# Kernel tuning notes

Hardware: AMD Instinct MI355X
Metric: run time of the kernel (lower is better)

## Reference

```python
import jax, jax.numpy as jnp
import numpy as np
from jax import lax

B, T, EPROJS, DUNITS, ATT_DIM = 32, 2048, 1024, 1024, 512
ACONV_CHANS, ACONV_FILTS = 32, 15
SCALING = 2.0


def setup_inputs() -> dict:
    key = jax.random.key(0)
    ks = jax.random.split(key, 12)
    enc_hs_pad = jax.random.normal(ks[0], (B, T, EPROJS), dtype=jnp.float32)
    enc_hs_len = jax.random.randint(ks[1], (B,), T // 2, T + 1, dtype=jnp.int32)
    dec_z = jax.random.normal(ks[2], (B, DUNITS), dtype=jnp.float32)
    ap = jax.random.uniform(ks[3], (B, T), dtype=jnp.float32)
    att_prev = ap / jnp.sum(ap, axis=1, keepdims=True)  # previous attention distribution
    # parameters (PyTorch Linear: y = x @ W^T + b; stored here pre-transposed as [in, out])
    s_enc = 1.0 / np.sqrt(EPROJS)
    s_dec = 1.0 / np.sqrt(DUNITS)
    s_att = 1.0 / np.sqrt(ACONV_CHANS)
    s_g = 1.0 / np.sqrt(ATT_DIM)
    K = 2 * ACONV_FILTS + 1
    s_c = 1.0 / np.sqrt(K)
    W_enc = jax.random.uniform(ks[4], (EPROJS, ATT_DIM), jnp.float32, -s_enc, s_enc)
    b_enc = jax.random.uniform(ks[5], (ATT_DIM,), jnp.float32, -s_enc, s_enc)
    W_dec = jax.random.uniform(ks[6], (DUNITS, ATT_DIM), jnp.float32, -s_dec, s_dec)
    W_att = jax.random.uniform(ks[7], (ACONV_CHANS, ATT_DIM), jnp.float32, -s_att, s_att)
    conv_w = jax.random.uniform(ks[8], (ACONV_CHANS, 1, K), jnp.float32, -s_c, s_c)
    W_g = jax.random.uniform(ks[9], (ATT_DIM, 1), jnp.float32, -s_g, s_g)
    b_g = jax.random.uniform(ks[10], (1,), jnp.float32, -s_g, s_g)
    return {"enc_hs_pad": enc_hs_pad, "enc_hs_len": enc_hs_len, "dec_z": dec_z,
            "att_prev": att_prev, "W_enc": W_enc, "b_enc": b_enc, "W_dec": W_dec,
            "W_att": W_att, "conv_w": conv_w, "W_g": W_g, "b_g": b_g}


def reference(enc_hs_pad, enc_hs_len, dec_z, att_prev,
              W_enc, b_enc, W_dec, W_att, conv_w, W_g, b_g):
    # pre-computed encoder projection: (B, T, A)
    pre_enc = jnp.einsum('btd,da->bta', enc_hs_pad, W_enc) + b_enc
    # location conv over previous attention: (B, 1, T) -> (B, C, T), SAME padding
    pad = (conv_w.shape[-1] - 1) // 2
    att_conv = lax.conv_general_dilated(
        att_prev[:, None, :], conv_w, window_strides=(1,),
        padding=[(pad, pad)], dimension_numbers=('NCH', 'OIH', 'NCH'))
    att_c = jnp.einsum('bct,ca->bta', att_conv, W_att)       # (B, T, A)
    dec_t = (dec_z @ W_dec)[:, None, :]                       # (B, 1, A)
    # energies: (B, T)
    e = jnp.einsum('bta,ao->bt', jnp.tanh(att_c + pre_enc + dec_t), W_g) + b_g[0]
    # pad mask: True where t >= length
    mask = jnp.arange(e.shape[1])[None, :] >= enc_hs_len[:, None]
    e = jnp.where(mask, -jnp.inf, e)
    w = jax.nn.softmax(SCALING * e, axis=1)                   # (B, T)
    c = jnp.einsum('btd,bt->bd', enc_hs_pad, w)               # (B, EPROJS)
    return c, w
```

## Files before the change

### kernel.cpp

```cpp
#include <hip/hip_runtime.h>
#include <stdint.h>

#define T_LEN 2048
#define KAUG  1056
#define M_TOT 65536

typedef __attribute__((ext_vector_type(8))) short short8;
typedef __attribute__((ext_vector_type(4))) float f32x4;
typedef unsigned int u32;
typedef unsigned short u16;

__device__ __forceinline__ u16 bf16_rn(float f){
  u32 u = __builtin_bit_cast(u32, f);
  u32 r = u + 0x7fffu + ((u >> 16) & 1u);
  return (u16)(r >> 16);
}
__device__ __forceinline__ u32 pack_trunc(float lo, float hi){
  u32 a = __builtin_bit_cast(u32, lo);
  u32 b = __builtin_bit_cast(u32, hi);
  return (a >> 16) | (b & 0xffff0000u);
}
__device__ __forceinline__ void lds_load16(const void* g, void* l){
  __builtin_amdgcn_global_load_lds(
      (const __attribute__((address_space(1))) u32*)g,
      (__attribute__((address_space(3))) u32*)l, 16, 0, 0);
}

__global__ void k_build_bt(const float* __restrict__ W_enc,
                           const float* __restrict__ W_att,
                           u16* __restrict__ Bt){
  __shared__ float tile[32][33];
  int k0 = blockIdx.x * 32, n0 = blockIdx.y * 32;
  int tx = threadIdx.x & 31, ty = threadIdx.x >> 5;
  #pragma unroll
  for (int i = 0; i < 4; i++){
    int k = k0 + i*8 + ty;
    int n = n0 + tx;
    float v = (k < 1024) ? W_enc[k*512 + n] : W_att[(k-1024)*512 + n];
    tile[i*8+ty][tx] = v;
  }
  __syncthreads();
  #pragma unroll
  for (int i = 0; i < 4; i++){
    int n = n0 + i*8 + ty;
    int k = k0 + tx;
    Bt[(size_t)n*KAUG + k] = bf16_rn(tile[tx][i*8+ty]);
  }
}

__global__ void k_bias(const float* __restrict__ dec_z,
                       const float* __restrict__ W_dec,
                       const float* __restrict__ b_enc,
                       float* __restrict__ bias){
  __shared__ float red[4][64];
  int b = blockIdx.y, n0 = blockIdx.x * 64;
  int nl = threadIdx.x & 63, ks = threadIdx.x >> 6;
  int n = n0 + nl;
  const float* dz = dec_z + b*1024;
  float s = 0.f;
  #pragma unroll 4
  for (int k = ks*256; k < ks*256 + 256; k++) s += dz[k] * W_dec[k*512 + n];
  red[ks][nl] = s;
  __syncthreads();
  if (threadIdx.x < 64){
    int nn = n0 + threadIdx.x;
    bias[b*512 + nn] = b_enc[nn] + red[0][threadIdx.x] + red[1][threadIdx.x]
                     + red[2][threadIdx.x] + red[3][threadIdx.x];
  }
}

__global__ void k_conv(const float* __restrict__ att_prev,
                       const float* __restrict__ conv_w,
                       float* __restrict__ attT){
  int idx = blockIdx.x*256 + threadIdx.x;
  int c = idx & 31;
  int bt = idx >> 5;
  int b = bt >> 11, t = bt & 2047;
  const float* ap = att_prev + b*2048;
  const float* cw = conv_w + c*31;
  float s = 0.f;
  #pragma unroll
  for (int j = 0; j < 31; j++){
    int tt = t + j - 15;
    float a = (tt >= 0 && tt < 2048) ? ap[tt] : 0.f;
    s += cw[j] * a;
  }
  attT[(size_t)bt*32 + c] = s;
}

__launch_bounds__(256)
__global__ void k_gemm_energy(const float* __restrict__ enc,
                              const float* __restrict__ attT,
                              const u16* __restrict__ Bt,
                              const float* __restrict__ bias,
                              const float* __restrict__ Wg,
                              float* __restrict__ ePart){
  __shared__ float Ash[128*32];
  __shared__ u16   Bsh[128*32];
  __shared__ float eRed[2][128];

  const int tid  = threadIdx.x;
  const int lane = tid & 63;
  const int wid  = tid >> 6;
  const int wave_m = wid >> 1, wave_n = wid & 1;
  const int bidx = blockIdx.x;
  const int xcd  = bidx & 7;
  const int s_sq = bidx >> 3;
  const int nblk = s_sq & 3;
  const int mblk = ((s_sq >> 2) << 3) + xcd;
  const int row0 = mblk << 7;
  const int b    = mblk >> 4;

  f32x4 acc[4][4];
  #pragma unroll
  for (int i = 0; i < 4; i++)
    #pragma unroll
    for (int j = 0; j < 4; j++) acc[i][j] = (f32x4)(0.f);

  const int arow_in = lane >> 3;
  const int ap_phys = lane & 7;
  const int brow_in = lane >> 2;
  const int bp_phys = lane & 3;
  const int fr_m = lane & 15;
  const int kg   = lane >> 4;

  const u16* BtN = Bt + (size_t)(nblk*128)*KAUG;

  #pragma unroll 1
  for (int kk = 0; kk < 33; ++kk){
    const float* srcA; int rstr;
    if (kk < 32){ srcA = enc  + (size_t)row0*1024 + kk*32; rstr = 1024; }
    else        { srcA = attT + (size_t)row0*32;           rstr = 32;   }
    #pragma unroll
    for (int q = 0; q < 4; q++){
      int r = wid*32 + q*8 + arow_in;
      int c = ap_phys ^ (r & 7);
      lds_load16(srcA + (size_t)r*rstr + c*4, Ash + (wid*32 + q*8)*32);
    }
    const u16* srcB = BtN + kk*32;
    #pragma unroll
    for (int q = 0; q < 2; q++){
      int n = wid*32 + q*16 + brow_in;
      int c = bp_phys ^ ((n >> 1) & 3);
      lds_load16(srcB + (size_t)n*KAUG + c*8, Bsh + (wid*32 + q*16)*32);
    }
    __syncthreads();

    short8 afrag[4], bfrag[4];
    #pragma unroll
    for (int mi = 0; mi < 4; mi++){
      int m  = wave_m*64 + mi*16 + fr_m;
      int c0 = kg*2;
      int p0 = c0 ^ (m & 7), p1 = (c0+1) ^ (m & 7);
      const f32x4* rowp = (const f32x4*)(Ash + m*32);
      f32x4 x0 = rowp[p0];
      f32x4 x1 = rowp[p1];
      union { u32 u[4]; short8 s; } cv;
      cv.u[0] = pack_trunc(x0.x, x0.y);
      cv.u[1] = pack_trunc(x0.z, x0.w);
      cv.u[2] = pack_trunc(x1.x, x1.y);
      cv.u[3] = pack_trunc(x1.z, x1.w);
      afrag[mi] = cv.s;
    }
    #pragma unroll
    for (int ni = 0; ni < 4; ni++){
      int n = wave_n*64 + ni*16 + fr_m;
      int p = kg ^ ((n >> 1) & 3);
      bfrag[ni] = *(const short8*)(Bsh + n*32 + p*8);
    }
    #pragma unroll
    for (int mi = 0; mi < 4; mi++)
      #pragma unroll
      for (int ni = 0; ni < 4; ni++)
        acc[mi][ni] = __builtin_amdgcn_mfma_f32_16x16x32_bf16(afrag[mi], bfrag[ni], acc[mi][ni], 0, 0, 0);

    __syncthreads();
  }

  float wg[4], bs[4];
  #pragma unroll
  for (int ni = 0; ni < 4; ni++){
    int ng = nblk*128 + wave_n*64 + ni*16 + fr_m;
    wg[ni] = Wg[ng];
    bs[ni] = bias[b*512 + ng];
  }
  #pragma unroll
  for (int mi = 0; mi < 4; mi++){
    #pragma unroll
    for (int reg = 0; reg < 4; reg++){
      float s = 0.f;
      #pragma unroll
      for (int ni = 0; ni < 4; ni++){
        float v  = acc[mi][ni][reg] + bs[ni];
        float e2 = __expf(2.f * v);
        float th = 1.f - 2.f/(e2 + 1.f);
        s += wg[ni] * th;
      }
      s += __shfl_xor(s, 1);
      s += __shfl_xor(s, 2);
      s += __shfl_xor(s, 4);
      s += __shfl_xor(s, 8);
      if (fr_m == 0){
        int rowl = wave_m*64 + mi*16 + kg*4 + reg;
        eRed[wave_n][rowl] = s;
      }
    }
  }
  __syncthreads();
  if (tid < 128)
    ePart[(size_t)nblk*M_TOT + row0 + tid] = eRed[0][tid] + eRed[1][tid];
}

__global__ void k_softmax(const float* __restrict__ ePart,
                          const int* __restrict__ lens,
                          float* __restrict__ wout){
  int b = blockIdx.x, tid = threadIdx.x;
  int lane = tid & 63, wid = tid >> 6;
  int len = lens[b];
  __shared__ float red[4];
  float x[8]; float m = -3.0e38f;
  #pragma unroll
  for (int i = 0; i < 8; i++){
    int t = tid + i*256;
    int idx = b*2048 + t;
    float e = ePart[idx] + ePart[M_TOT + idx] + ePart[2*M_TOT + idx] + ePart[3*M_TOT + idx];
    float xx = (t < len) ? 2.0f*e : -3.0e38f;
    x[i] = xx; m = fmaxf(m, xx);
  }
  #pragma unroll
  for (int o = 1; o < 64; o <<= 1) m = fmaxf(m, __shfl_xor(m, o));
  if (lane == 0) red[wid] = m;
  __syncthreads();
  m = fmaxf(fmaxf(red[0], red[1]), fmaxf(red[2], red[3]));
  float s = 0.f;
  #pragma unroll
  for (int i = 0; i < 8; i++){
    float ex = (x[i] > -1.0e38f) ? __expf(x[i] - m) : 0.f;
    x[i] = ex; s += ex;
  }
  #pragma unroll
  for (int o = 1; o < 64; o <<= 1) s += __shfl_xor(s, o);
  __syncthreads();
  if (lane == 0) red[wid] = s;
  __syncthreads();
  s = red[0] + red[1] + red[2] + red[3];
  float inv = 1.0f / s;
  #pragma unroll
  for (int i = 0; i < 8; i++){
    int t = tid + i*256;
    wout[b*2048 + t] = x[i]*inv;
  }
}

__global__ void k_ctx_partial(const float* __restrict__ enc,
                              const float* __restrict__ w,
                              float* __restrict__ cPart){
  int dc = blockIdx.x, tc = blockIdx.y, b = blockIdx.z;
  int d = dc*256 + threadIdx.x;
  const float* ep = enc + ((size_t)(b*2048 + tc*256))*1024 + d;
  const float* wp = w + b*2048 + tc*256;
  float s0 = 0, s1 = 0, s2 = 0, s3 = 0;
  #pragma unroll 2
  for (int t = 0; t < 256; t += 4){
    s0 += wp[t+0] * ep[(size_t)(t+0)*1024];
    s1 += wp[t+1] * ep[(size_t)(t+1)*1024];
    s2 += wp[t+2] * ep[(size_t)(t+2)*1024];
    s3 += wp[t+3] * ep[(size_t)(t+3)*1024];
  }
  cPart[((size_t)tc*32 + b)*1024 + d] = (s0 + s1) + (s2 + s3);
}

__global__ void k_ctx_reduce(const float* __restrict__ cPart, float* __restrict__ cOut){
  int idx = blockIdx.x*256 + threadIdx.x;
  float s = 0.f;
  #pragma unroll
  for (int tc = 0; tc < 8; tc++) s += cPart[tc*32768 + idx];
  cOut[idx] = s;
}

extern "C" void kernel_launch(void* const* d_in, const int* in_sizes, int n_in,
                              void* d_out, int out_size, void* d_ws, size_t ws_size,
                              hipStream_t stream){
  (void)in_sizes; (void)n_in; (void)out_size; (void)ws_size;
  const float* enc    = (const float*)d_in[0];
  const int*   lens   = (const int*)  d_in[1];
  const float* dec_z  = (const float*)d_in[2];
  const float* att_p  = (const float*)d_in[3];
  const float* W_enc  = (const float*)d_in[4];
  const float* b_enc  = (const float*)d_in[5];
  const float* W_dec  = (const float*)d_in[6];
  const float* W_att  = (const float*)d_in[7];
  const float* conv_w = (const float*)d_in[8];
  const float* W_g    = (const float*)d_in[9];

  char* ws = (char*)d_ws;
  u16*   Bt    = (u16*)  (ws);
  float* attT  = (float*)(ws + 1081344);
  float* bias  = (float*)(ws + 1081344 + 8388608);
  float* ePart = (float*)(ws + 1081344 + 8388608 + 65536);
  float* cPart = (float*)(ws + 1081344 + 8388608 + 65536 + 1048576);

  float* c_out = (float*)d_out;
  float* w_out = c_out + 32*1024;

  hipLaunchKernelGGL(k_build_bt,    dim3(33,16),  dim3(256), 0, stream, W_enc, W_att, Bt);
  hipLaunchKernelGGL(k_bias,        dim3(8,32),   dim3(256), 0, stream, dec_z, W_dec, b_enc, bias);
  hipLaunchKernelGGL(k_conv,        dim3(8192),   dim3(256), 0, stream, att_p, conv_w, attT);
  hipLaunchKernelGGL(k_gemm_energy, dim3(2048),   dim3(256), 0, stream, enc, attT, Bt, bias, W_g, ePart);
  hipLaunchKernelGGL(k_softmax,     dim3(32),     dim3(256), 0, stream, ePart, lens, w_out);
  hipLaunchKernelGGL(k_ctx_partial, dim3(4,8,32), dim3(256), 0, stream, enc, w_out, cPart);
  hipLaunchKernelGGL(k_ctx_reduce,  dim3(128),    dim3(256), 0, stream, cPart, c_out);
}
```

Measured before the change: 594.3 us.

## Pre-convert encoder states to bf16 and fuse conv features into augmented rows

Adds a pass that converts the encoder tensor to bf16 into a workspace buffer, with the location-conv outputs written into the extra 32 columns of each row. The GEMM then stages bf16 A tiles directly via LDS loads instead of loading f32 and truncating per fragment. The context kernel is vectorized to float4 with more time chunks. This adds an extra full read/write pass over the encoder tensor and requires a large workspace, falling back to the old f32 path otherwise.

After: 655.2 us. +10.3%, slower.

```diff
diff --git a/kernel.cpp b/kernel.cpp
--- a/kernel.cpp
+++ b/kernel.cpp
@@ -3,6 +3,7 @@
 
 #define T_LEN 2048
 #define KAUG  1056
+#define ROWB  1056
 #define M_TOT 65536
 
 typedef __attribute__((ext_vector_type(8))) short short8;
@@ -44,7 +45,7 @@
   for (int i = 0; i < 4; i++){
     int n = n0 + i*8 + ty;
     int k = k0 + tx;
-    Bt[(size_t)n*KAUG + k] = bf16_rn(tile[tx][i*8+ty]);
+    Bt[(size_t)n*ROWB + k] = bf16_rn(tile[tx][i*8+ty]);
   }
 }
 
@@ -69,9 +70,20 @@
   }
 }
 
-__global__ void k_conv(const float* __restrict__ att_prev,
-                       const float* __restrict__ conv_w,
-                       float* __restrict__ attT){
+__global__ void k_cvt(const float* __restrict__ enc, u16* __restrict__ encB){
+  int g = blockIdx.x*256 + threadIdx.x;
+  int bt = g >> 7, kx = (g & 127) << 3;
+  const f32x4* in = (const f32x4*)(enc + (size_t)bt*1024 + kx);
+  f32x4 a = in[0], b = in[1];
+  union { u16 h[8]; uint4 v; } o;
+  o.h[0]=bf16_rn(a.x); o.h[1]=bf16_rn(a.y); o.h[2]=bf16_rn(a.z); o.h[3]=bf16_rn(a.w);
+  o.h[4]=bf16_rn(b.x); o.h[5]=bf16_rn(b.y); o.h[6]=bf16_rn(b.z); o.h[7]=bf16_rn(b.w);
+  *(uint4*)(encB + (size_t)bt*ROWB + kx) = o.v;
+}
+
+__global__ void k_conv_bf16(const float* __restrict__ att_prev,
+                            const float* __restrict__ conv_w,
+                            u16* __restrict__ encB){
   int idx = blockIdx.x*256 + threadIdx.x;
   int c = idx & 31;
   int bt = idx >> 5;
@@ -85,18 +97,36 @@
     float a = (tt >= 0 && tt < 2048) ? ap[tt] : 0.f;
     s += cw[j] * a;
   }
+  encB[(size_t)bt*ROWB + 1024 + c] = bf16_rn(s);
+}
+
+__global__ void k_conv_f32(const float* __restrict__ att_prev,
+                           const float* __restrict__ conv_w,
+                           float* __restrict__ attT){
+  int idx = blockIdx.x*256 + threadIdx.x;
+  int c = idx & 31;
+  int bt = idx >> 5;
+  int b = bt >> 11, t = bt & 2047;
+  const float* ap = att_prev + b*2048;
+  const float* cw = conv_w + c*31;
+  float s = 0.f;
+  #pragma unroll
+  for (int j = 0; j < 31; j++){
+    int tt = t + j - 15;
+    float a = (tt >= 0 && tt < 2048) ? ap[tt] : 0.f;
+    s += cw[j] * a;
+  }
   attT[(size_t)bt*32 + c] = s;
 }
 
 __launch_bounds__(256)
-__global__ void k_gemm_energy(const float* __restrict__ enc,
-                              const float* __restrict__ attT,
-                              const u16* __restrict__ Bt,
-                              const float* __restrict__ bias,
-                              const float* __restrict__ Wg,
-                              float* __restrict__ ePart){
-  __shared__ float Ash[128*32];
-  __shared__ u16   Bsh[128*32];
+__global__ void k_gemm_bf16(const u16* __restrict__ encB,
+                            const u16* __restrict__ Bt,
+                            const float* __restrict__ bias,
+                            const float* __restrict__ Wg,
+                            float* __restrict__ ePart){
+  __shared__ u16 Ash[128*32];
+  __shared__ u16 Bsh[128*32];
   __shared__ float eRed[2][128];
 
   const int tid  = threadIdx.x;
@@ -117,50 +147,32 @@
     #pragma unroll
     for (int j = 0; j < 4; j++) acc[i][j] = (f32x4)(0.f);
 
-  const int arow_in = lane >> 3;
-  const int ap_phys = lane & 7;
-  const int brow_in = lane >> 2;
-  const int bp_phys = lane & 3;
+  const int r_in = lane >> 2;
+  const int phys = lane & 3;
   const int fr_m = lane & 15;
   const int kg   = lane >> 4;
 
-  const u16* BtN = Bt + (size_t)(nblk*128)*KAUG;
+  const u16* Abase = encB + (size_t)row0*ROWB;
+  const u16* Bbase = Bt + (size_t)(nblk*128)*ROWB;
 
   #pragma unroll 1
   for (int kk = 0; kk < 33; ++kk){
-    const float* srcA; int rstr;
-    if (kk < 32){ srcA = enc  + (size_t)row0*1024 + kk*32; rstr = 1024; }
-    else        { srcA = attT + (size_t)row0*32;           rstr = 32;   }
-    #pragma unroll
-    for (int q = 0; q < 4; q++){
-      int r = wid*32 + q*8 + arow_in;
-      int c = ap_phys ^ (r & 7);
-      lds_load16(srcA + (size_t)r*rstr + c*4, Ash + (wid*32 + q*8)*32);
-    }
-    const u16* srcB = BtN + kk*32;
+    const int k0 = kk*32;
     #pragma unroll
     for (int q = 0; q < 2; q++){
-      int n = wid*32 + q*16 + brow_in;
-      int c = bp_phys ^ ((n >> 1) & 3);
-      lds_load16(srcB + (size_t)n*KAUG + c*8, Bsh + (wid*32 + q*16)*32);
+      int r = q*64 + wid*16 + r_in;
+      int c = phys ^ ((r >> 1) & 3);
+      lds_load16(Abase + (size_t)r*ROWB + k0 + c*8, Ash + (q*64 + wid*16)*32);
+      lds_load16(Bbase + (size_t)r*ROWB + k0 + c*8, Bsh + (q*64 + wid*16)*32);
     }
     __syncthreads();
 
     short8 afrag[4], bfrag[4];
     #pragma unroll
     for (int mi = 0; mi < 4; mi++){
-      int m  = wave_m*64 + mi*16 + fr_m;
-      int c0 = kg*2;
-      int p0 = c0 ^ (m & 7), p1 = (c0+1) ^ (m & 7);
-      const f32x4* rowp = (const f32x4*)(Ash + m*32);
-      f32x4 x0 = rowp[p0];
-      f32x4 x1 = rowp[p1];
-      union { u32 u[4]; short8 s; } cv;
-      cv.u[0] = pack_trunc(x0.x, x0.y);
-      cv.u[1] = pack_trunc(x0.z, x0.w);
-      cv.u[2] = pack_trunc(x1.x, x1.y);
-      cv.u[3] = pack_trunc(x1.z, x1.w);
-      afrag[mi] = cv.s;
+      int m = wave_m*64 + mi*16 + fr_m;
+      int p = kg ^ ((m >> 1) & 3);
+      afrag[mi] = *(const short8*)(Ash + m*32 + p*8);
     }
     #pragma unroll
     for (int ni = 0; ni < 4; ni++){
@@ -211,6 +223,129 @@
     ePart[(size_t)nblk*M_TOT + row0 + tid] = eRed[0][tid] + eRed[1][tid];
 }
 
+__launch_bounds__(256)
+__global__ void k_gemm_f32(const float* __restrict__ enc,
+                           const float* __restrict__ attT,
+                           const u16* __restrict__ Bt,
+                           const float* __restrict__ bias,
+                           const float* __restrict__ Wg,
+                           float* __restrict__ ePart){
+  __shared__ float Ash[128*32];
+  __shared__ u16   Bsh[128*32];
+  __shared__ float eRed[2][128];
+
+  const int tid  = threadIdx.x;
+  const int lane = tid & 63;
+  const int wid  = tid >> 6;
+  const int wave_m = wid >> 1, wave_n = wid & 1;
+  const int bidx = blockIdx.x;
+  const int xcd  = bidx & 7;
+  const int s_sq = bidx >> 3;
+  const int nblk = s_sq & 3;
+  const int mblk = ((s_sq >> 2) << 3) + xcd;
+  const int row0 = mblk << 7;
+  const int b    = mblk >> 4;
+
+  f32x4 acc[4][4];
+  #pragma unroll
+  for (int i = 0; i < 4; i++)
+    #pragma unroll
+    for (int j = 0; j < 4; j++) acc[i][j] = (f32x4)(0.f);
+
+  const int arow_in = lane >> 3;
+  const int ap_phys = lane & 7;
+  const int brow_in = lane >> 2;
+  const int bp_phys = lane & 3;
+  const int fr_m = lane & 15;
+  const int kg   = lane >> 4;
+
+  const u16* BtN = Bt + (size_t)(nblk*128)*ROWB;
+
+  #pragma unroll 1
+  for (int kk = 0; kk < 33; ++kk){
+    const float* srcA; int rstr;
+    if (kk < 32){ srcA = enc  + (size_t)row0*1024 + kk*32; rstr = 1024; }
+    else        { srcA = attT + (size_t)row0*32;           rstr = 32;   }
+    #pragma unroll
+    for (int q = 0; q < 4; q++){
+      int r = wid*32 + q*8 + arow_in;
+      int c = ap_phys ^ (r & 7);
+      lds_load16(srcA + (size_t)r*rstr + c*4, Ash + (wid*32 + q*8)*32);
+    }
+    const u16* srcB = BtN + kk*32;
+    #pragma unroll
+    for (int q = 0; q < 2; q++){
+      int n = wid*32 + q*16 + brow_in;
+      int c = bp_phys ^ ((n >> 1) & 3);
+      lds_load16(srcB + (size_t)n*ROWB + c*8, Bsh + (wid*32 + q*16)*32);
+    }
+    __syncthreads();
+
+    short8 afrag[4], bfrag[4];
+    #pragma unroll
+    for (int mi = 0; mi < 4; mi++){
+      int m  = wave_m*64 + mi*16 + fr_m;
+      int c0 = kg*2;
+      int p0 = c0 ^ (m & 7), p1 = (c0+1) ^ (m & 7);
+      const f32x4* rowp = (const f32x4*)(Ash + m*32);
+      f32x4 x0 = rowp[p0];
+      f32x4 x1 = rowp[p1];
+      union { u32 u[4]; short8 s; } cv;
+      cv.u[0] = pack_trunc(x0.x, x0.y);
+      cv.u[1] = pack_trunc(x0.z, x0.w);
+      cv.u[2] = pack_trunc(x1.x, x1.y);
+      cv.u[3] = pack_trunc(x1.z, x1.w);
+      afrag[mi] = cv.s;
+    }
+    #pragma unroll
+    for (int ni = 0; ni < 4; ni++){
+      int n = wave_n*64 + ni*16 + fr_m;
+      int p = kg ^ ((n >> 1) & 3);
+      bfrag[ni] = *(const short8*)(Bsh + n*32 + p*8);
+    }
+    #pragma unroll
+    for (int mi = 0; mi < 4; mi++)
+      #pragma unroll
+      for (int ni = 0; ni < 4; ni++)
+        acc[mi][ni] = __builtin_amdgcn_mfma_f32_16x16x32_bf16(afrag[mi], bfrag[ni], acc[mi][ni], 0, 0, 0);
+
+    __syncthreads();
+  }
+
+  float wg[4], bs[4];
+  #pragma unroll
+  for (int ni = 0; ni < 4; ni++){
+    int ng = nblk*128 + wave_n*64 + ni*16 + fr_m;
+    wg[ni] = Wg[ng];
+    bs[ni] = bias[b*512 + ng];
+  }
+  #pragma unroll
+  for (int mi = 0; mi < 4; mi++){
+    #pragma unroll
+    for (int reg = 0; reg < 4; reg++){
+      float s = 0.f;
+      #pragma unroll
+      for (int ni = 0; ni < 4; ni++){
+        float v  = acc[mi][ni][reg] + bs[ni];
+        float e2 = __expf(2.f * v);
+        float th = 1.f - 2.f/(e2 + 1.f);
+        s += wg[ni] * th;
+      }
+      s += __shfl_xor(s, 1);
+      s += __shfl_xor(s, 2);
+      s += __shfl_xor(s, 4);
+      s += __shfl_xor(s, 8);
+      if (fr_m == 0){
+        int rowl = wave_m*64 + mi*16 + kg*4 + reg;
+        eRed[wave_n][rowl] = s;
+      }
+    }
+  }
+  __syncthreads();
+  if (tid < 128)
+    ePart[(size_t)nblk*M_TOT + row0 + tid] = eRed[0][tid] + eRed[1][tid];
+}
+
 __global__ void k_softmax(const float* __restrict__ ePart,
                           const int* __restrict__ lens,
                           float* __restrict__ wout){
@@ -255,33 +390,35 @@
 __global__ void k_ctx_partial(const float* __restrict__ enc,
                               const float* __restrict__ w,
                               float* __restrict__ cPart){
-  int dc = blockIdx.x, tc = blockIdx.y, b = blockIdx.z;
-  int d = dc*256 + threadIdx.x;
-  const float* ep = enc + ((size_t)(b*2048 + tc*256))*1024 + d;
-  const float* wp = w + b*2048 + tc*256;
-  float s0 = 0, s1 = 0, s2 = 0, s3 = 0;
+  int tc = blockIdx.x;
+  int b  = blockIdx.y;
+  int d4 = threadIdx.x;
+  const f32x4* ep = (const f32x4*)(enc + ((size_t)(b*2048 + tc*128))*1024) + d4;
+  const float* wp = w + b*2048 + tc*128;
+  f32x4 a0 = (f32x4)(0.f), a1 = (f32x4)(0.f), a2 = (f32x4)(0.f), a3 = (f32x4)(0.f);
   #pragma unroll 2
-  for (int t = 0; t < 256; t += 4){
-    s0 += wp[t+0] * ep[(size_t)(t+0)*1024];
-    s1 += wp[t+1] * ep[(size_t)(t+1)*1024];
-    s2 += wp[t+2] * ep[(size_t)(t+2)*1024];
-    s3 += wp[t+3] * ep[(size_t)(t+3)*1024];
-  }
-  cPart[((size_t)tc*32 + b)*1024 + d] = (s0 + s1) + (s2 + s3);
+  for (int t = 0; t < 128; t += 4){
+    a0 += wp[t+0] * ep[(size_t)(t+0)*256];
+    a1 += wp[t+1] * ep[(size_t)(t+1)*256];
+    a2 += wp[t+2] * ep[(size_t)(t+2)*256];
+    a3 += wp[t+3] * ep[(size_t)(t+3)*256];
+  }
+  f32x4 r = (a0 + a1) + (a2 + a3);
+  *(f32x4*)(cPart + ((size_t)tc*32 + b)*1024 + d4*4) = r;
 }
 
 __global__ void k_ctx_reduce(const float* __restrict__ cPart, float* __restrict__ cOut){
   int idx = blockIdx.x*256 + threadIdx.x;
   float s = 0.f;
   #pragma unroll
-  for (int tc = 0; tc < 8; tc++) s += cPart[tc*32768 + idx];
+  for (int tc = 0; tc < 16; tc++) s += cPart[(size_t)tc*32768 + idx];
   cOut[idx] = s;
 }
 
 extern "C" void kernel_launch(void* const* d_in, const int* in_sizes, int n_in,
                               void* d_out, int out_size, void* d_ws, size_t ws_size,
                               hipStream_t stream){
-  (void)in_sizes; (void)n_in; (void)out_size; (void)ws_size;
+  (void)in_sizes; (void)n_in; (void)out_size;
   const float* enc    = (const float*)d_in[0];
   const int*   lens   = (const int*)  d_in[1];
   const float* dec_z  = (const float*)d_in[2];
@@ -293,21 +430,32 @@
   const float* conv_w = (const float*)d_in[8];
   const float* W_g    = (const float*)d_in[9];
 
+  float* c_out = (float*)d_out;
+  float* w_out = c_out + 32*1024;
+
   char* ws = (char*)d_ws;
   u16*   Bt    = (u16*)  (ws);
-  float* attT  = (float*)(ws + 1081344);
-  float* bias  = (float*)(ws + 1081344 + 8388608);
-  float* ePart = (float*)(ws + 1081344 + 8388608 + 65536);
-  float* cPart = (float*)(ws + 1081344 + 8388608 + 65536 + 1048576);
-
-  float* c_out = (float*)d_out;
-  float* w_out = c_out + 32*1024;
-
-  hipLaunchKernelGGL(k_build_bt,    dim3(33,16),  dim3(256), 0, stream, W_enc, W_att, Bt);
-  hipLaunchKernelGGL(k_bias,        dim3(8,32),   dim3(256), 0, stream, dec_z, W_dec, b_enc, bias);
-  hipLaunchKernelGGL(k_conv,        dim3(8192),   dim3(256), 0, stream, att_p, conv_w, attT);
-  hipLaunchKernelGGL(k_gemm_energy, dim3(2048),   dim3(256), 0, stream, enc, attT, Bt, bias, W_g, ePart);
+  float* bias  = (float*)(ws + 1081344);
+  float* ePart = (float*)(ws + 1146880);
+  float* cPart = (float*)(ws + 2195456);
+
+  const size_t need_fast = 4292608ull + 138412032ull;
+
+  hipLaunchKernelGGL(k_build_bt, dim3(33,16), dim3(256), 0, stream, W_enc, W_att, Bt);
+  hipLaunchKernelGGL(k_bias,     dim3(8,32),  dim3(256), 0, stream, dec_z, W_dec, b_enc, bias);
+
+  if (ws_size >= need_fast){
+    u16* encB = (u16*)(ws + 4292608);
+    hipLaunchKernelGGL(k_cvt,       dim3(32768), dim3(256), 0, stream, enc, encB);
+    hipLaunchKernelGGL(k_conv_bf16, dim3(8192),  dim3(256), 0, stream, att_p, conv_w, encB);
+    hipLaunchKernelGGL(k_gemm_bf16, dim3(2048),  dim3(256), 0, stream, encB, Bt, bias, W_g, ePart);
+  } else {
+    float* attT = (float*)(ws + 4292608);
+    hipLaunchKernelGGL(k_conv_f32,  dim3(8192),  dim3(256), 0, stream, att_p, conv_w, attT);
+    hipLaunchKernelGGL(k_gemm_f32,  dim3(2048),  dim3(256), 0, stream, enc, attT, Bt, bias, W_g, ePart);
+  }
+
   hipLaunchKernelGGL(k_softmax,     dim3(32),     dim3(256), 0, stream, ePart, lens, w_out);
-  hipLaunchKernelGGL(k_ctx_partial, dim3(4,8,32), dim3(256), 0, stream, enc, w_out, cPart);
+  hipLaunchKernelGGL(k_ctx_partial, dim3(16,32),  dim3(256), 0, stream, enc, w_out, cPart);
   hipLaunchKernelGGL(k_ctx_reduce,  dim3(128),    dim3(256), 0, stream, cPart, c_out);
 }
```
